# Performance work log

Hardware: AMD Instinct MI355X
Metric: run time of the kernel (lower is better)

The kernel has to match this reference:

```python
import jax, jax.numpy as jnp
import numpy as np

NQ, NT, D = 2048, 131072, 64   # query nodes, target nodes, feature dim
E = 2_000_000                  # candidate (u, v) edges
M = 1024                       # consensus (nn_map) pairs; vc = top M rows of Xt


def setup_inputs() -> dict:
    key = jax.random.key(0)
    ks = jax.random.split(key, 8)
    Xq = jax.random.normal(ks[0], (NQ, D), dtype=jnp.float32)
    Xt = jax.random.normal(ks[1], (NT, D), dtype=jnp.float32)
    W_alpha = jax.random.normal(ks[2], (D, D), dtype=jnp.float32) * 0.05
    b_alpha = jax.random.normal(ks[3], (1,), dtype=jnp.float32) * 0.05
    W_beta = jax.random.normal(ks[4], (D, D), dtype=jnp.float32) * 0.05
    b_beta = jax.random.normal(ks[5], (1,), dtype=jnp.float32) * 0.05
    u_idx = jax.random.randint(ks[6], (E,), 0, NQ, dtype=jnp.int32)
    # candidate targets live in [0, NT - M); consensus targets in [NT - M, NT)
    v_idx = jax.random.randint(ks[7], (E,), 0, NT - M, dtype=jnp.int32)
    uc = jax.random.randint(jax.random.fold_in(key, 7), (M,), 0, NQ, dtype=jnp.int32)
    vc = (NT - M) + jnp.arange(M, dtype=jnp.int32)
    return {"Xq": Xq, "Xt": Xt, "W_alpha": W_alpha, "b_alpha": b_alpha,
            "W_beta": W_beta, "b_beta": b_beta,
            "u_idx": u_idx, "v_idx": v_idx, "uc": uc, "vc": vc}


def reference(Xq, Xt, W_alpha, b_alpha, W_beta, b_beta, u_idx, v_idx, uc, vc):
    # 1) consensus overwrite: Xt[vc] = Xq[uc]  (nn_map)
    Xt_c = Xt.at[vc].set(Xq[uc])

    # 2) per-edge gather + bilinear interaction scoring
    xq_e = Xq[u_idx]      # [E, D]
    xt_e = Xt_c[v_idx]    # [E, D]

    def bilinear(W, b):
        return jnp.einsum('ed,df,ef->e', xq_e, W, xt_e) + b[0]

    beta = jax.nn.sigmoid(bilinear(W_beta, b_beta))   # [E] gate
    alpha = jax.nn.elu(bilinear(W_alpha, b_alpha))    # [E] score
    h_e = (1.0 - beta)[:, None] * xq_e + beta[:, None] * xt_e  # [E, D]

    # 3) segment softmax over incoming u per target v (== masked softmax over Nq)
    m = jax.ops.segment_max(alpha, v_idx, num_segments=NT)     # -inf on empty segments
    a = jnp.exp(alpha - m[v_idx])
    s = jax.ops.segment_sum(a, v_idx, num_segments=NT)
    a = a / s[v_idx] + 1e-10   # matches original +1e-10 after normalization

    # 4) scatter-aggregate weighted messages back into Xt rows with >=1 candidate
    agg = jax.ops.segment_sum(a[:, None] * h_e, v_idx, num_segments=NT)  # [NT, D]
    deg = jax.ops.segment_sum(jnp.ones_like(alpha), v_idx, num_segments=NT)
    Xt_out = jnp.where((deg > 0)[:, None], agg, Xt_c)
    return (Xq, Xt_out)
```

## Files before the change

kernel.cpp:

```cpp
#include <hip/hip_runtime.h>

#define NQ 2048
#define NT 131072
#define DD 64
#define MM 1024
#define NBUCK 512
#define BCAP 4608
#define CHUNK 4096

__global__ void yq_kernel(const float* __restrict__ Xq,
                          const float* __restrict__ Wa,
                          const float* __restrict__ Wb,
                          float* __restrict__ Yqa,
                          float* __restrict__ Yqb) {
    int r = blockIdx.x * 4 + (threadIdx.x >> 6);
    int j = threadIdx.x & 63;
    float sa = 0.f, sb = 0.f;
#pragma unroll
    for (int k = 0; k < DD; ++k) {
        float x = Xq[r * DD + k];
        sa = fmaf(x, Wa[k * DD + j], sa);
        sb = fmaf(x, Wb[k * DD + j], sb);
    }
    Yqa[r * DD + j] = sa;
    Yqb[r * DD + j] = sb;
}

__global__ __launch_bounds__(1024) void bin_kernel(
        const int* __restrict__ u_idx, const int* __restrict__ v_idx,
        int* __restrict__ gcur, unsigned* __restrict__ gbuf, int E) {
    __shared__ unsigned stage[CHUNK];
    __shared__ int hist[NBUCK], off[NBUCK], base[NBUCK], cur[NBUCK];
    int tid = threadIdx.x;
    int e0 = blockIdx.x * CHUNK;
    int n = min(CHUNK, E - e0);
    if (n <= 0) return;

    for (int i = tid; i < NBUCK; i += 1024) hist[i] = 0;
    __syncthreads();

    unsigned p[4];
    int nv = 0;
    int i0 = tid * 4;
    if (i0 + 3 < n) {
        int4 u4 = *(const int4*)(u_idx + e0 + i0);
        int4 v4 = *(const int4*)(v_idx + e0 + i0);
        p[0] = ((unsigned)v4.x << 11) | (unsigned)u4.x;
        p[1] = ((unsigned)v4.y << 11) | (unsigned)u4.y;
        p[2] = ((unsigned)v4.z << 11) | (unsigned)u4.z;
        p[3] = ((unsigned)v4.w << 11) | (unsigned)u4.w;
        nv = 4;
    } else {
        for (int j = 0; j < 4; ++j) {
            if (i0 + j < n) {
                p[j] = ((unsigned)v_idx[e0 + i0 + j] << 11) | (unsigned)u_idx[e0 + i0 + j];
                ++nv;
            }
        }
    }
    for (int j = 0; j < nv; ++j) atomicAdd(&hist[p[j] >> 19], 1);
    __syncthreads();
    if (tid < 64) {
        int h[8], sum = 0;
#pragma unroll
        for (int j = 0; j < 8; ++j) { h[j] = hist[8 * tid + j]; sum += h[j]; }
        int incl = sum;
#pragma unroll
        for (int d = 1; d < 64; d <<= 1) {
            int y = __shfl_up(incl, d, 64);
            if (tid >= d) incl += y;
        }
        int excl = incl - sum;
#pragma unroll
        for (int j = 0; j < 8; ++j) { off[8 * tid + j] = excl; excl += h[j]; }
    }
    __syncthreads();
    for (int i = tid; i < NBUCK; i += 1024) {
        base[i] = hist[i] ? atomicAdd(&gcur[i], hist[i]) : 0;
        cur[i] = off[i];
    }
    __syncthreads();
    for (int j = 0; j < nv; ++j) {
        int pos = atomicAdd(&cur[p[j] >> 19], 1);
        stage[pos] = p[j];
    }
    __syncthreads();
    for (int i = tid; i < n; i += 1024) {
        unsigned q = stage[i];
        int b = q >> 19;
        int idx = base[b] + (i - off[b]);
        if (idx < BCAP) gbuf[(size_t)b * BCAP + idx] = q;
    }
}

#define DOT4(a, b) fmaf((a).x, (b).x, fmaf((a).y, (b).y, fmaf((a).z, (b).z, (a).w * (b).w)))

__global__ __launch_bounds__(1024, 2) void bucket_kernel(
        const float* __restrict__ Xq,
        const float* __restrict__ Xt,
        const float* __restrict__ Yqa,
        const float* __restrict__ Yqb,
        const float* __restrict__ ba,
        const float* __restrict__ bb,
        const int* __restrict__ gcur,
        const unsigned* __restrict__ gbuf,
        const int* __restrict__ uc,
        float* __restrict__ outXt) {
    __shared__ unsigned short su[BCAP];
    __shared__ int hist[256], cur[256], rstart[257];
    int tid = threadIdx.x;
    int b = blockIdx.x;
    int n = min(gcur[b], BCAP);

    if (tid < 256) hist[tid] = 0;
    __syncthreads();
    for (int i = tid; i < n; i += 1024)
        atomicAdd(&hist[(gbuf[(size_t)b * BCAP + i] >> 11) & 255], 1);
    __syncthreads();
    if (tid < 64) {
        int h0 = hist[4 * tid], h1 = hist[4 * tid + 1];
        int h2 = hist[4 * tid + 2], h3 = hist[4 * tid + 3];
        int tot = h0 + h1 + h2 + h3;
        int incl = tot;
#pragma unroll
        for (int d = 1; d < 64; d <<= 1) {
            int y = __shfl_up(incl, d, 64);
            if (tid >= d) incl += y;
        }
        int excl = incl - tot;
        rstart[4 * tid] = excl;             cur[4 * tid] = excl;
        rstart[4 * tid + 1] = excl + h0;    cur[4 * tid + 1] = excl + h0;
        rstart[4 * tid + 2] = excl + h0 + h1;      cur[4 * tid + 2] = excl + h0 + h1;
        rstart[4 * tid + 3] = excl + h0 + h1 + h2; cur[4 * tid + 3] = excl + h0 + h1 + h2;
        if (tid == 63) rstart[256] = excl + tot;
    }
    __syncthreads();
    for (int i = tid; i < n; i += 1024) {
        unsigned p = gbuf[(size_t)b * BCAP + i];
        int pos = atomicAdd(&cur[(p >> 11) & 255], 1);
        su[pos] = (unsigned short)(p & 0x7FFu);
    }
    __syncthreads();

    int lane = tid & 63;
    int w = tid >> 6;
    int l16 = lane & 15;
    int g = lane >> 4;
    int gid = w * 4 + g;
    float ba0 = ba[0], bb0 = bb[0];

    for (int r = gid; r < 256; r += 64) {
        int v = (b << 8) + r;
        int startr = rstart[r];
        int deg = rstart[r + 1] - startr;
        if (deg == 0) {
            float4 o;
            if (v >= NT - MM) {
                int u = uc[v - (NT - MM)];
                o = ((const float4*)(Xq + (size_t)u * DD))[l16];
            } else {
                o = ((const float4*)(Xt + (size_t)v * DD))[l16];
            }
            ((float4*)(outXt + (size_t)v * DD))[l16] = o;
            continue;
        }
        float4 xt4 = ((const float4*)(Xt + (size_t)v * DD))[l16];
        float4 acc = make_float4(0.f, 0.f, 0.f, 0.f);
        float s = 0.f;
        int k = 0;
        for (; k + 1 < deg; k += 2) {
            int u0 = (int)su[startr + k];
            int u1 = (int)su[startr + k + 1];
            float4 ya0 = ((const float4*)(Yqa + u0 * DD))[l16];
            float4 yb0 = ((const float4*)(Yqb + u0 * DD))[l16];
            float4 ya1 = ((const float4*)(Yqa + u1 * DD))[l16];
            float4 yb1 = ((const float4*)(Yqb + u1 * DD))[l16];
            float pa0 = DOT4(ya0, xt4), pb0 = DOT4(yb0, xt4);
            float pa1 = DOT4(ya1, xt4), pb1 = DOT4(yb1, xt4);
#pragma unroll
            for (int off = 1; off < 16; off <<= 1) {
                pa0 += __shfl_xor(pa0, off, 64);
                pb0 += __shfl_xor(pb0, off, 64);
                pa1 += __shfl_xor(pa1, off, 64);
                pb1 += __shfl_xor(pb1, off, 64);
            }
            float la0 = pa0 + ba0, la1 = pa1 + ba0;
            float t0 = __expf(la0), t1 = __expf(la1);
            float al0 = la0 > 0.f ? la0 : (t0 - 1.f);
            float al1 = la1 > 0.f ? la1 : (t1 - 1.f);
            float a0 = __expf(al0), a1 = __expf(al1);
            float be0 = __builtin_amdgcn_rcpf(1.f + __expf(-(pb0 + bb0)));
            float be1 = __builtin_amdgcn_rcpf(1.f + __expf(-(pb1 + bb0)));
            float4 xq0 = ((const float4*)(Xq + u0 * DD))[l16];
            float4 xq1 = ((const float4*)(Xq + u1 * DD))[l16];
            float4 h0, h1;
            h0.x = fmaf(be0, xt4.x - xq0.x, xq0.x);
            h0.y = fmaf(be0, xt4.y - xq0.y, xq0.y);
            h0.z = fmaf(be0, xt4.z - xq0.z, xq0.z);
            h0.w = fmaf(be0, xt4.w - xq0.w, xq0.w);
            h1.x = fmaf(be1, xt4.x - xq1.x, xq1.x);
            h1.y = fmaf(be1, xt4.y - xq1.y, xq1.y);
            h1.z = fmaf(be1, xt4.z - xq1.z, xq1.z);
            h1.w = fmaf(be1, xt4.w - xq1.w, xq1.w);
            acc.x = fmaf(a0, h0.x, fmaf(a1, h1.x, acc.x));
            acc.y = fmaf(a0, h0.y, fmaf(a1, h1.y, acc.y));
            acc.z = fmaf(a0, h0.z, fmaf(a1, h1.z, acc.z));
            acc.w = fmaf(a0, h0.w, fmaf(a1, h1.w, acc.w));
            s += a0 + a1;
        }
        if (k < deg) {
            int u = (int)su[startr + k];
            float4 ya = ((const float4*)(Yqa + u * DD))[l16];
            float4 yb = ((const float4*)(Yqb + u * DD))[l16];
            float pa = DOT4(ya, xt4), pb = DOT4(yb, xt4);
#pragma unroll
            for (int off = 1; off < 16; off <<= 1) {
                pa += __shfl_xor(pa, off, 64);
                pb += __shfl_xor(pb, off, 64);
            }
            float la = pa + ba0;
            float t = __expf(la);
            float al = la > 0.f ? la : (t - 1.f);
            float a = __expf(al);
            float be = __builtin_amdgcn_rcpf(1.f + __expf(-(pb + bb0)));
            float4 xq = ((const float4*)(Xq + u * DD))[l16];
            acc.x = fmaf(a, fmaf(be, xt4.x - xq.x, xq.x), acc.x);
            acc.y = fmaf(a, fmaf(be, xt4.y - xq.y, xq.y), acc.y);
            acc.z = fmaf(a, fmaf(be, xt4.z - xq.z, xq.z), acc.z);
            acc.w = fmaf(a, fmaf(be, xt4.w - xq.w, xq.w), acc.w);
            s += a;
        }
        float inv = __builtin_amdgcn_rcpf(s);
        float4 o = make_float4(acc.x * inv, acc.y * inv, acc.z * inv, acc.w * inv);
        ((float4*)(outXt + (size_t)v * DD))[l16] = o;
    }
}

extern "C" void kernel_launch(void* const* d_in, const int* in_sizes, int n_in,
                              void* d_out, int out_size, void* d_ws, size_t ws_size,
                              hipStream_t stream) {
    const float* Xq = (const float*)d_in[0];
    const float* Xt = (const float*)d_in[1];
    const float* Wa = (const float*)d_in[2];
    const float* ba = (const float*)d_in[3];
    const float* Wb = (const float*)d_in[4];
    const float* bb = (const float*)d_in[5];
    const int* u_idx = (const int*)d_in[6];
    const int* v_idx = (const int*)d_in[7];
    const int* uc = (const int*)d_in[8];
    const int* vc = (const int*)d_in[9];
    const int E = in_sizes[6];
    (void)vc;

    float* out = (float*)d_out;
    float* outXq = out;
    float* outXt = out + NQ * DD;

    char* ws = (char*)d_ws;
    float* Yqa = (float*)ws;          ws += NQ * DD * sizeof(float);
    float* Yqb = (float*)ws;          ws += NQ * DD * sizeof(float);
    int* gcur = (int*)ws;             ws += NBUCK * sizeof(int);
    ws = (char*)(((size_t)ws + 255) & ~(size_t)255);
    unsigned* gbuf = (unsigned*)ws;   ws += (size_t)NBUCK * BCAP * sizeof(unsigned);

    hipMemcpyAsync(outXq, Xq, NQ * DD * sizeof(float), hipMemcpyDeviceToDevice, stream);
    hipMemsetAsync(gcur, 0, NBUCK * sizeof(int), stream);

    yq_kernel<<<NQ / 4, 256, 0, stream>>>(Xq, Wa, Wb, Yqa, Yqb);

    int nchunks = (E + CHUNK - 1) / CHUNK;
    bin_kernel<<<nchunks, 1024, 0, stream>>>(u_idx, v_idx, gcur, gbuf, E);

    bucket_kernel<<<NBUCK, 1024, 0, stream>>>(Xq, Xt, Yqa, Yqb, ba, bb, gcur, gbuf,
                                              uc, outXt);
}
```

Before: 218.3 us.

## Assign one wavefront per target row, split edges across quarter-waves, use DPP reductions

The bucket kernel now gives each target row a whole 64-lane wavefront instead of a 16-lane group. The four 16-lane groups each process different edges, eight per iteration, and their partial accumulators are combined with cross-group shuffles at the end. The Yqa/Yqb projections are interleaved into a single Yab array so each edge reads them from one contiguous row, and the 16-lane dot-product reductions use DPP row ops instead of ds_swizzle shuffles. This adds parallelism per row, which matters given the average degree of about 15, at the cost of masked lanes when degree isn't a multiple of 8. Zero-degree rows now leave three quarters of the wave idle.

Measured after the change: 226.1 us. +3.6%, slower.

```diff
diff --git a/kernel.cpp b/kernel.cpp
--- a/kernel.cpp
+++ b/kernel.cpp
@@ -11,8 +11,7 @@
 __global__ void yq_kernel(const float* __restrict__ Xq,
                           const float* __restrict__ Wa,
                           const float* __restrict__ Wb,
-                          float* __restrict__ Yqa,
-                          float* __restrict__ Yqb) {
+                          float* __restrict__ Yab) {
     int r = blockIdx.x * 4 + (threadIdx.x >> 6);
     int j = threadIdx.x & 63;
     float sa = 0.f, sb = 0.f;
@@ -22,8 +21,8 @@
         sa = fmaf(x, Wa[k * DD + j], sa);
         sb = fmaf(x, Wb[k * DD + j], sb);
     }
-    Yqa[r * DD + j] = sa;
-    Yqb[r * DD + j] = sb;
+    Yab[r * 2 * DD + j] = sa;
+    Yab[r * 2 * DD + DD + j] = sb;
 }
 
 __global__ __launch_bounds__(1024) void bin_kernel(
@@ -95,11 +94,24 @@
 
 #define DOT4(a, b) fmaf((a).x, (b).x, fmaf((a).y, (b).y, fmaf((a).z, (b).z, (a).w * (b).w)))
 
+template <int CTRL>
+__device__ __forceinline__ float dpp_add(float x) {
+    int xi = __builtin_bit_cast(int, x);
+    int yi = __builtin_amdgcn_update_dpp(xi, xi, CTRL, 0xF, 0xF, false);
+    return x + __builtin_bit_cast(float, yi);
+}
+__device__ __forceinline__ float red16(float x) {
+    x = dpp_add<0xB1>(x);
+    x = dpp_add<0x4E>(x);
+    x = dpp_add<0x124>(x);
+    x = dpp_add<0x128>(x);
+    return x;
+}
+
 __global__ __launch_bounds__(1024, 2) void bucket_kernel(
         const float* __restrict__ Xq,
         const float* __restrict__ Xt,
-        const float* __restrict__ Yqa,
-        const float* __restrict__ Yqb,
+        const float* __restrict__ Yab,
         const float* __restrict__ ba,
         const float* __restrict__ bb,
         const int* __restrict__ gcur,
@@ -146,53 +158,52 @@
     int w = tid >> 6;
     int l16 = lane & 15;
     int g = lane >> 4;
-    int gid = w * 4 + g;
     float ba0 = ba[0], bb0 = bb[0];
 
-    for (int r = gid; r < 256; r += 64) {
+    for (int r = w; r < 256; r += 16) {
         int v = (b << 8) + r;
         int startr = rstart[r];
         int deg = rstart[r + 1] - startr;
         if (deg == 0) {
-            float4 o;
-            if (v >= NT - MM) {
-                int u = uc[v - (NT - MM)];
-                o = ((const float4*)(Xq + (size_t)u * DD))[l16];
-            } else {
-                o = ((const float4*)(Xt + (size_t)v * DD))[l16];
+            if (g == 0) {
+                float4 o;
+                if (v >= NT - MM) {
+                    int u = uc[v - (NT - MM)];
+                    o = ((const float4*)(Xq + (size_t)u * DD))[l16];
+                } else {
+                    o = ((const float4*)(Xt + (size_t)v * DD))[l16];
+                }
+                ((float4*)(outXt + (size_t)v * DD))[l16] = o;
             }
-            ((float4*)(outXt + (size_t)v * DD))[l16] = o;
             continue;
         }
         float4 xt4 = ((const float4*)(Xt + (size_t)v * DD))[l16];
         float4 acc = make_float4(0.f, 0.f, 0.f, 0.f);
         float s = 0.f;
-        int k = 0;
-        for (; k + 1 < deg; k += 2) {
-            int u0 = (int)su[startr + k];
-            int u1 = (int)su[startr + k + 1];
-            float4 ya0 = ((const float4*)(Yqa + u0 * DD))[l16];
-            float4 yb0 = ((const float4*)(Yqb + u0 * DD))[l16];
-            float4 ya1 = ((const float4*)(Yqa + u1 * DD))[l16];
-            float4 yb1 = ((const float4*)(Yqb + u1 * DD))[l16];
+        for (int base = 0; base < deg; base += 8) {
+            int e0 = base + g;
+            int e1 = base + 4 + g;
+            bool ok0 = e0 < deg, ok1 = e1 < deg;
+            int u0 = (int)su[startr + (ok0 ? e0 : 0)];
+            int u1 = (int)su[startr + (ok1 ? e1 : 0)];
+            const float4* Y0 = (const float4*)(Yab + u0 * (2 * DD));
+            const float4* Y1 = (const float4*)(Yab + u1 * (2 * DD));
+            float4 ya0 = Y0[l16], yb0 = Y0[16 + l16];
+            float4 ya1 = Y1[l16], yb1 = Y1[16 + l16];
             float pa0 = DOT4(ya0, xt4), pb0 = DOT4(yb0, xt4);
             float pa1 = DOT4(ya1, xt4), pb1 = DOT4(yb1, xt4);
-#pragma unroll
-            for (int off = 1; off < 16; off <<= 1) {
-                pa0 += __shfl_xor(pa0, off, 64);
-                pb0 += __shfl_xor(pb0, off, 64);
-                pa1 += __shfl_xor(pa1, off, 64);
-                pb1 += __shfl_xor(pb1, off, 64);
-            }
+            pa0 = red16(pa0); pb0 = red16(pb0);
+            pa1 = red16(pa1); pb1 = red16(pb1);
             float la0 = pa0 + ba0, la1 = pa1 + ba0;
             float t0 = __expf(la0), t1 = __expf(la1);
             float al0 = la0 > 0.f ? la0 : (t0 - 1.f);
             float al1 = la1 > 0.f ? la1 : (t1 - 1.f);
-            float a0 = __expf(al0), a1 = __expf(al1);
+            float a0 = ok0 ? __expf(al0) : 0.f;
+            float a1 = ok1 ? __expf(al1) : 0.f;
             float be0 = __builtin_amdgcn_rcpf(1.f + __expf(-(pb0 + bb0)));
             float be1 = __builtin_amdgcn_rcpf(1.f + __expf(-(pb1 + bb0)));
-            float4 xq0 = ((const float4*)(Xq + u0 * DD))[l16];
-            float4 xq1 = ((const float4*)(Xq + u1 * DD))[l16];
+            float4 xq0 = ((const float4*)(Xq + (size_t)u0 * DD))[l16];
+            float4 xq1 = ((const float4*)(Xq + (size_t)u1 * DD))[l16];
             float4 h0, h1;
             h0.x = fmaf(be0, xt4.x - xq0.x, xq0.x);
             h0.y = fmaf(be0, xt4.y - xq0.y, xq0.y);
@@ -208,31 +219,21 @@
             acc.w = fmaf(a0, h0.w, fmaf(a1, h1.w, acc.w));
             s += a0 + a1;
         }
-        if (k < deg) {
-            int u = (int)su[startr + k];
-            float4 ya = ((const float4*)(Yqa + u * DD))[l16];
-            float4 yb = ((const float4*)(Yqb + u * DD))[l16];
-            float pa = DOT4(ya, xt4), pb = DOT4(yb, xt4);
-#pragma unroll
-            for (int off = 1; off < 16; off <<= 1) {
-                pa += __shfl_xor(pa, off, 64);
-                pb += __shfl_xor(pb, off, 64);
-            }
-            float la = pa + ba0;
-            float t = __expf(la);
-            float al = la > 0.f ? la : (t - 1.f);
-            float a = __expf(al);
-            float be = __builtin_amdgcn_rcpf(1.f + __expf(-(pb + bb0)));
-            float4 xq = ((const float4*)(Xq + u * DD))[l16];
-            acc.x = fmaf(a, fmaf(be, xt4.x - xq.x, xq.x), acc.x);
-            acc.y = fmaf(a, fmaf(be, xt4.y - xq.y, xq.y), acc.y);
-            acc.z = fmaf(a, fmaf(be, xt4.z - xq.z, xq.z), acc.z);
-            acc.w = fmaf(a, fmaf(be, xt4.w - xq.w, xq.w), acc.w);
-            s += a;
-        }
-        float inv = __builtin_amdgcn_rcpf(s);
-        float4 o = make_float4(acc.x * inv, acc.y * inv, acc.z * inv, acc.w * inv);
-        ((float4*)(outXt + (size_t)v * DD))[l16] = o;
+        acc.x += __shfl_xor(acc.x, 16, 64);
+        acc.y += __shfl_xor(acc.y, 16, 64);
+        acc.z += __shfl_xor(acc.z, 16, 64);
+        acc.w += __shfl_xor(acc.w, 16, 64);
+        s     += __shfl_xor(s, 16, 64);
+        acc.x += __shfl_xor(acc.x, 32, 64);
+        acc.y += __shfl_xor(acc.y, 32, 64);
+        acc.z += __shfl_xor(acc.z, 32, 64);
+        acc.w += __shfl_xor(acc.w, 32, 64);
+        s     += __shfl_xor(s, 32, 64);
+        if (g == 0) {
+            float inv = __builtin_amdgcn_rcpf(s);
+            float4 o = make_float4(acc.x * inv, acc.y * inv, acc.z * inv, acc.w * inv);
+            ((float4*)(outXt + (size_t)v * DD))[l16] = o;
+        }
     }
 }
 
@@ -257,8 +258,7 @@
     float* outXt = out + NQ * DD;
 
     char* ws = (char*)d_ws;
-    float* Yqa = (float*)ws;          ws += NQ * DD * sizeof(float);
-    float* Yqb = (float*)ws;          ws += NQ * DD * sizeof(float);
+    float* Yab = (float*)ws;          ws += (size_t)NQ * 2 * DD * sizeof(float);
     int* gcur = (int*)ws;             ws += NBUCK * sizeof(int);
     ws = (char*)(((size_t)ws + 255) & ~(size_t)255);
     unsigned* gbuf = (unsigned*)ws;   ws += (size_t)NBUCK * BCAP * sizeof(unsigned);
@@ -266,11 +266,11 @@
     hipMemcpyAsync(outXq, Xq, NQ * DD * sizeof(float), hipMemcpyDeviceToDevice, stream);
     hipMemsetAsync(gcur, 0, NBUCK * sizeof(int), stream);
 
-    yq_kernel<<<NQ / 4, 256, 0, stream>>>(Xq, Wa, Wb, Yqa, Yqb);
+    yq_kernel<<<NQ / 4, 256, 0, stream>>>(Xq, Wa, Wb, Yab);
 
     int nchunks = (E + CHUNK - 1) / CHUNK;
     bin_kernel<<<nchunks, 1024, 0, stream>>>(u_idx, v_idx, gcur, gbuf, E);
 
-    bucket_kernel<<<NBUCK, 1024, 0, stream>>>(Xq, Xt, Yqa, Yqb, ba, bb, gcur, gbuf,
+    bucket_kernel<<<NBUCK, 1024, 0, stream>>>(Xq, Xt, Yab, ba, bb, gcur, gbuf,
                                               uc, outXt);
 }
```
